# Kernel tuning notes

Hardware: AMD Instinct MI355X
Metric: run time of the kernel (lower is better)

## Reference

```python
import jax, jax.numpy as jnp
import numpy as np

ALPHA = 0.8  # STE clipping threshold (unused in fwd-only path)


def binary_sign(x):
    # torch: x.sign() with zeros mapped to +1 => where(x >= 0, 1, -1)
    return jnp.where(x >= 0, jnp.ones((), x.dtype), -jnp.ones((), x.dtype))


def setup_inputs() -> dict:
    key = jax.random.key(0)
    ks = jax.random.split(key, 5)
    B, D = 16384, 4096
    x = jax.random.normal(ks[0], (B, D), dtype=jnp.float32)
    w0 = jax.random.normal(ks[1], (D, D), dtype=jnp.float32) * 0.1
    w1 = jax.random.normal(ks[2], (D, D), dtype=jnp.float32) * 0.1
    w2 = jax.random.normal(ks[3], (D, D), dtype=jnp.float32) * 0.1
    w3 = jax.random.normal(ks[4], (1, D), dtype=jnp.float32) * 0.1
    b0 = jnp.zeros((D,), jnp.float32)
    b1 = jnp.zeros((D,), jnp.float32)
    b2 = jnp.zeros((D,), jnp.float32)
    b3 = jnp.zeros((1,), jnp.float32)
    return {"x": x, "w0": w0, "b0": b0, "w1": w1, "b1": b1,
            "w2": w2, "b2": b2, "w3": w3, "b3": b3}


def reference(x, w0, b0, w1, b1, w2, b2, w3, b3):
    h = x
    for w, b in ((w0, b0), (w1, b1), (w2, b2), (w3, b3)):
        # BinaryLinear: binarize weights, dense matmul, add bias
        z = jnp.einsum('bi,oi->bo', h, binary_sign(w)) + b
        # BinaryActivation: binarize pre-activation
        h = binary_sign(z)
    return h  # [B, 1]
```

## Files before the change

### kernel.cpp

```cpp
#include <hip/hip_runtime.h>

typedef int   v4i  __attribute__((ext_vector_type(4)));
typedef int   v16i __attribute__((ext_vector_type(16)));
typedef float f4   __attribute__((ext_vector_type(4)));

#define DD 4096
#define BATCH 16384

__device__ __forceinline__ void gload16(const void* g, void* l) {
  __builtin_amdgcn_global_load_lds((const __attribute__((address_space(1))) void*)g,
                                   (__attribute__((address_space(3))) void*)l, 16, 0, 0);
}
#define ASM_VMCNT(n) asm volatile("s_waitcnt vmcnt(" #n ")" ::: "memory")
#define ASM_LGKM0()  asm volatile("s_waitcnt lgkmcnt(0)" ::: "memory")
#define BARF()       asm volatile("s_barrier" ::: "memory")


__global__ void binarize_swz_k(const float* __restrict__ w, unsigned char* __restrict__ o,
                               int swz_on) {
  int T = blockIdx.x * blockDim.x + threadIdx.x;
  int row = T >> 10, rem = T & 1023;
  int kblk = rem >> 4, seg = (rem >> 2) & 3, q = rem & 3;
  f4 v = *(const f4*)(w + (size_t)row * DD + kblk * 64 + seg * 16 + q * 4);
  unsigned int r = 0;
#pragma unroll
  for (int j = 0; j < 4; ++j) {
    unsigned int b = (v[j] >= 0.0f) ? 0x01u : 0xFFu;
    r |= b << (8 * j);
  }
  int slot = swz_on ? (seg ^ ((row >> 1) & 3)) : seg;
  *(unsigned int*)(o + (size_t)row * DD + kblk * 64 + slot * 16 + q * 4) = r;
}

__global__ void rowsum_k(const unsigned char* __restrict__ wb, int* __restrict__ R) {
  int lane = threadIdx.x & 63, wid = threadIdx.x >> 6;
  int row = blockIdx.x * 4 + wid;
  const unsigned char* p = wb + (size_t)row * DD;
  int s = 0;
#pragma unroll
  for (int j = 0; j < 4; ++j) {
    v4i a = *(const v4i*)(p + lane * 16 + j * 1024);
#pragma unroll
    for (int w = 0; w < 4; ++w) {
      unsigned int xa = (unsigned int)a[w];
#pragma unroll
      for (int by = 0; by < 4; ++by)
        s += (int)(signed char)((xa >> (8 * by)) & 255u);
    }
  }
#pragma unroll
  for (int off = 32; off > 0; off >>= 1) s += __shfl_down(s, off);
  if (lane == 0) R[row] = s;
}

__global__ void digitize_k(const float* __restrict__ x, unsigned char* __restrict__ Xd) {
  int T = blockIdx.x * blockDim.x + threadIdx.x;
  int row = T >> 10, rem = T & 1023;
  int kblk = rem >> 4, seg = (rem >> 2) & 3, q = rem & 3;
  f4 v = *(const f4*)(x + (size_t)row * DD + kblk * 64 + seg * 16 + q * 4);
  unsigned int Y[4];
#pragma unroll
  for (int j = 0; j < 4; ++j) {
    int X = (int)(v[j] * 134217728.0f);
    Y[j] = (unsigned int)(X + 1073741824);
  }
  size_t base = (size_t)row * 16384 + (size_t)kblk * 256;
  int r7 = row & 7;
#pragma unroll
  for (int d = 0; d < 4; ++d) {
    unsigned int wv = ((Y[0] >> (8 * d)) & 255u)
                    | (((Y[1] >> (8 * d)) & 255u) << 8)
                    | (((Y[2] >> (8 * d)) & 255u) << 16)
                    | (((Y[3] >> (8 * d)) & 255u) << 24);
    wv ^= 0x80808080u;
    int slot = ((d << 2) | seg) ^ r7;
    *(unsigned int*)(Xd + base + slot * 16 + q * 4) = wv;
  }
}

__global__ __launch_bounds__(256, 2) void gemm0p_k(
    const unsigned char* __restrict__ Xd, const unsigned char* __restrict__ wb,
    const int* __restrict__ R, const float* __restrict__ bias,
    signed char* __restrict__ h1) {
  __shared__ unsigned char As[2][64 * 256];
  __shared__ unsigned char Bs[2][128 * 64];
  const int tid = threadIdx.x, lane = tid & 63, wid = tid >> 6;
  const int wm = wid >> 1, wn = wid & 1;
  const int bid = blockIdx.x;
  const int xcd = bid & 7, sl = bid >> 3;
  const int m0 = ((xcd << 5) + (sl >> 5)) << 6;
  const int n0 = (sl & 31) << 7;

  v16i acc[4][2];
#pragma unroll
  for (int d = 0; d < 4; ++d)
#pragma unroll
    for (int f = 0; f < 2; ++f)
#pragma unroll
      for (int e = 0; e < 16; ++e) acc[d][f][e] = 0;

  auto stage = [&](int bf, int kb) {
#pragma unroll
    for (int i = 0; i < 4; ++i) {
      int c = wid * 4 + i;
      int lrow = c * 4 + (lane >> 4);
      const unsigned char* g = Xd + (size_t)(m0 + lrow) * 16384 + (size_t)kb * 256 + (lane & 15) * 16;
      gload16(g, &As[bf][c * 1024]);
    }
#pragma unroll
    for (int j = 0; j < 2; ++j) {
      int c = wid * 2 + j;
      int lrowB = c * 16 + (lane >> 2);
      const unsigned char* gB = wb + (size_t)(n0 + lrowB) * 4096 + kb * 64 + (lane & 3) * 16;
      gload16(gB, &Bs[bf][c * 1024]);
    }
  };

  const int rl = lane & 31, hi = lane >> 5;
  const int arow = wm * 32 + rl;
  const int r7 = arow & 7;

  stage(0, 0);
  stage(1, 1);
  ASM_VMCNT(6); BARF();
  int cur = 0;
  for (int t = 0; t < 64; ++t) {
    v4i af[2][4], bg[2][2];
#pragma unroll
    for (int kt = 0; kt < 2; ++kt) {
      int g = kt * 2 + hi;
#pragma unroll
      for (int d = 0; d < 4; ++d) {
        int slot = ((d << 2) | g) ^ r7;
        af[kt][d] = *(const v4i*)&As[cur][arow * 256 + slot * 16];
      }
#pragma unroll
      for (int f = 0; f < 2; ++f) {
        int brow = wn * 64 + f * 32 + rl;
        int slotb = g ^ ((brow >> 1) & 3);
        bg[kt][f] = *(const v4i*)&Bs[cur][brow * 64 + slotb * 16];
      }
    }
    ASM_LGKM0(); BARF();
    if (t < 62) stage(cur, t + 2);
    __builtin_amdgcn_s_setprio(1);
#pragma unroll
    for (int kt = 0; kt < 2; ++kt)
#pragma unroll
      for (int d = 0; d < 4; ++d)
#pragma unroll
        for (int f = 0; f < 2; ++f)
          acc[d][f] = __builtin_amdgcn_mfma_i32_32x32x32_i8(af[kt][d], bg[kt][f], acc[d][f], 0, 0, 0);
    __builtin_amdgcn_s_setprio(0);
    if (t < 62) { ASM_VMCNT(6); BARF(); }
    else if (t == 62) { ASM_VMCNT(0); BARF(); }
    cur ^= 1;
  }

#pragma unroll
  for (int f = 0; f < 2; ++f) {
    int col = n0 + wn * 64 + f * 32 + (lane & 31);
    long long rterm = 1082163328LL * (long long)R[col];
    double bb = (double)bias[col];
#pragma unroll
    for (int r = 0; r < 16; ++r) {
      long long Z = (long long)acc[0][f][r] + 256LL * (long long)acc[1][f][r]
                  + 65536LL * (long long)acc[2][f][r] + 16777216LL * (long long)acc[3][f][r]
                  + rterm;
      double z = (double)Z * 7.450580596923828125e-9 + bb;
      int row = m0 + wm * 32 + (r & 3) + 8 * (r >> 2) + 4 * (lane >> 5);
      int col2 = col ^ (((row >> 1) & 3) << 4);
      h1[(size_t)row * DD + col2] = (z >= 0.0) ? (signed char)1 : (signed char)(-1);
    }
  }
}

__global__ __launch_bounds__(512, 2) void gemm0f_k(
    const float* __restrict__ x, const unsigned char* __restrict__ wb,
    const int* __restrict__ R, const float* __restrict__ bias,
    signed char* __restrict__ h1) {
  __shared__ signed char As[2][4][128 * 80];
  __shared__ signed char Bs[2][128 * 80];
  const int tid = threadIdx.x;
  const int lane = tid & 63, wid = tid >> 6;
  const int wm = wid >> 1, wn = wid & 1;
  const int n0 = blockIdx.x * 128, m0 = blockIdx.y * 128;

  v16i acc[4][2];
#pragma unroll
  for (int d = 0; d < 4; ++d)
#pragma unroll
    for (int f = 0; f < 2; ++f)
#pragma unroll
      for (int e = 0; e < 16; ++e) acc[d][f][e] = 0;

  const int arow_l = tid >> 4, aseg = tid & 15;
  const int brow = tid >> 2,  bseg = (tid & 3) * 16;
  f4 va[4]; v4i vb;

  auto loadTile = [&](int kpos) {
#pragma unroll
    for (int p = 0; p < 4; ++p)
      va[p] = *(const f4*)(x + (size_t)(m0 + p * 32 + arow_l) * DD + kpos + aseg * 4);
    vb = *(const v4i*)(wb + (size_t)(n0 + brow) * DD + kpos + bseg);
  };
  auto writeTile = [&](int bf) {
#pragma unroll
    for (int p = 0; p < 4; ++p) {
      int row = p * 32 + arow_l;
      unsigned int Y[4];
#pragma unroll
      for (int j = 0; j < 4; ++j) {
        int X = (int)(va[p][j] * 134217728.0f);
        Y[j] = (unsigned int)(X + 1073741824);
      }
#pragma unroll
      for (int k = 0; k < 4; ++k) {
        unsigned int wv = ((Y[0] >> (8 * k)) & 255u) | (((Y[1] >> (8 * k)) & 255u) << 8)
                        | (((Y[2] >> (8 * k)) & 255u) << 16) | (((Y[3] >> (8 * k)) & 255u) << 24);
        wv ^= 0x80808080u;
        *(unsigned int*)&As[bf][k][row * 80 + aseg * 4] = wv;
      }
    }
    *(v4i*)&Bs[bf][brow * 80 + bseg] = vb;
  };

  loadTile(0); writeTile(0);
  __syncthreads();
  for (int t = 0; t < 64; ++t) {
    int cur = t & 1;
    if (t < 63) loadTile((t + 1) * 64);
#pragma unroll
    for (int kt = 0; kt < 2; ++kt) {
      int g = kt * 2 + (lane >> 5);
      int ar = (wm * 32 + (lane & 31)) * 80 + g * 16;
      v4i a[4], b[2];
#pragma unroll
      for (int d = 0; d < 4; ++d) a[d] = *(const v4i*)&As[cur][d][ar];
#pragma unroll
      for (int f = 0; f < 2; ++f) {
        int br = wn * 64 + f * 32 + (lane & 31);
        int slotb = g ^ ((br >> 1) & 3);
        b[f] = *(const v4i*)&Bs[cur][br * 80 + slotb * 16];
      }
#pragma unroll
      for (int d = 0; d < 4; ++d)
#pragma unroll
        for (int f = 0; f < 2; ++f)
          acc[d][f] = __builtin_amdgcn_mfma_i32_32x32x32_i8(a[d], b[f], acc[d][f], 0, 0, 0);
    }
    if (t < 63) writeTile(cur ^ 1);
    __syncthreads();
  }

#pragma unroll
  for (int f = 0; f < 2; ++f) {
    int col = n0 + wn * 64 + f * 32 + (lane & 31);
    long long rterm = 1082163328LL * (long long)R[col];
    double bb = (double)bias[col];
#pragma unroll
    for (int r = 0; r < 16; ++r) {
      long long Z = (long long)acc[0][f][r] + 256LL * (long long)acc[1][f][r]
                  + 65536LL * (long long)acc[2][f][r] + 16777216LL * (long long)acc[3][f][r]
                  + rterm;
      double z = (double)Z * 7.450580596923828125e-9 + bb;
      int row = m0 + wm * 32 + (r & 3) + 8 * (r >> 2) + 4 * (lane >> 5);
      int col2 = col ^ (((row >> 1) & 3) << 4);
      h1[(size_t)row * DD + col2] = (z >= 0.0) ? (signed char)1 : (signed char)(-1);
    }
  }
}

__global__ __launch_bounds__(256, 3) void gemm_bin_k(
    const unsigned char* __restrict__ A, const unsigned char* __restrict__ Bw,
    const float* __restrict__ bias, signed char* __restrict__ out) {
  __shared__ unsigned char As[2][128 * 64];
  __shared__ unsigned char Bs[2][128 * 64];
  const int tid = threadIdx.x, lane = tid & 63, wid = tid >> 6;
  const int wm = wid >> 1, wn = wid & 1;
  const int bid = blockIdx.x;
  const int xcd = bid & 7, sl = bid >> 3;
  const int m0 = ((xcd << 4) + (sl >> 5)) << 7;
  const int n0 = (sl & 31) << 7;

  v16i acc[2][2];
#pragma unroll
  for (int mi = 0; mi < 2; ++mi)
#pragma unroll
    for (int f = 0; f < 2; ++f)
#pragma unroll
      for (int e = 0; e < 16; ++e) acc[mi][f][e] = 0;

  auto stage = [&](int bf, int kb) {
#pragma unroll
    for (int j = 0; j < 2; ++j) {
      int c = wid * 2 + j;
      int lrow = c * 16 + (lane >> 2);
      const unsigned char* gA = A  + (size_t)(m0 + lrow) * 4096 + kb * 64 + (lane & 3) * 16;
      const unsigned char* gB = Bw + (size_t)(n0 + lrow) * 4096 + kb * 64 + (lane & 3) * 16;
      gload16(gA, &As[bf][c * 1024]);
      gload16(gB, &Bs[bf][c * 1024]);
    }
  };

  const int rl = lane & 31, hi = lane >> 5;

  stage(0, 0);
  stage(1, 1);
  ASM_VMCNT(4); BARF();
  int cur = 0;
  for (int t = 0; t < 64; ++t) {
    v4i af[2][2], bg[2][2];
#pragma unroll
    for (int kt = 0; kt < 2; ++kt) {
      int g = kt * 2 + hi;
#pragma unroll
      for (int mi = 0; mi < 2; ++mi) {
        int arow = wm * 64 + mi * 32 + rl;
        int slot = g ^ ((arow >> 1) & 3);
        af[kt][mi] = *(const v4i*)&As[cur][arow * 64 + slot * 16];
      }
#pragma unroll
      for (int f = 0; f < 2; ++f) {
        int brow = wn * 64 + f * 32 + rl;
        int slot = g ^ ((brow >> 1) & 3);
        bg[kt][f] = *(const v4i*)&Bs[cur][brow * 64 + slot * 16];
      }
    }
    ASM_LGKM0(); BARF();
    if (t < 62) stage(cur, t + 2);
    __builtin_amdgcn_s_setprio(1);
#pragma unroll
    for (int kt = 0; kt < 2; ++kt)
#pragma unroll
      for (int mi = 0; mi < 2; ++mi)
#pragma unroll
        for (int f = 0; f < 2; ++f)
          acc[mi][f] = __builtin_amdgcn_mfma_i32_32x32x32_i8(af[kt][mi], bg[kt][f], acc[mi][f], 0, 0, 0);
    __builtin_amdgcn_s_setprio(0);
    if (t < 62) { ASM_VMCNT(4); BARF(); }
    else if (t == 62) { ASM_VMCNT(0); BARF(); }
    cur ^= 1;
  }

#pragma unroll
  for (int mi = 0; mi < 2; ++mi)
#pragma unroll
    for (int f = 0; f < 2; ++f) {
      int col = n0 + wn * 64 + f * 32 + (lane & 31);
      float bb = bias[col];
#pragma unroll
      for (int r = 0; r < 16; ++r) {
        float z = (float)acc[mi][f][r] + bb;
        int row = m0 + wm * 64 + mi * 32 + (r & 3) + 8 * (r >> 2) + 4 * (lane >> 5);
        int col2 = col ^ (((row >> 1) & 3) << 4);
        out[(size_t)row * DD + col2] = (z >= 0.0f) ? (signed char)1 : (signed char)(-1);
      }
    }
}

__global__ void final_k(const unsigned char* __restrict__ h, const unsigned char* __restrict__ w3b,
                        const float* __restrict__ b3, float* __restrict__ out) {
  int lane = threadIdx.x & 63, wid = threadIdx.x >> 6;
  int row = blockIdx.x * 4 + wid;
  int swz = ((row >> 1) & 3) << 4;
  const unsigned char* p = h + (size_t)row * DD;
  int s = 0;
#pragma unroll
  for (int j = 0; j < 4; ++j) {
    int e = lane * 16 + j * 1024;
    v4i a = *(const v4i*)(p + (e ^ swz));
    v4i b = *(const v4i*)(w3b + e);
#pragma unroll
    for (int w = 0; w < 4; ++w) {
      unsigned int xa = (unsigned int)a[w], xb = (unsigned int)b[w];
#pragma unroll
      for (int by = 0; by < 4; ++by)
        s += (int)(signed char)((xa >> (8 * by)) & 255u)
           * (int)(signed char)((xb >> (8 * by)) & 255u);
    }
  }
#pragma unroll
  for (int off = 32; off > 0; off >>= 1) s += __shfl_down(s, off);
  if (lane == 0) {
    float z = (float)s + b3[0];
    out[row] = (z >= 0.0f) ? 1.0f : -1.0f;
  }
}

extern "C" void kernel_launch(void* const* d_in, const int* in_sizes, int n_in,
                              void* d_out, int out_size, void* d_ws, size_t ws_size,
                              hipStream_t stream) {
  (void)in_sizes; (void)n_in; (void)out_size;
  const float* x  = (const float*)d_in[0];
  const float* w0 = (const float*)d_in[1];
  const float* b0 = (const float*)d_in[2];
  const float* w1 = (const float*)d_in[3];
  const float* b1 = (const float*)d_in[4];
  const float* w2 = (const float*)d_in[5];
  const float* b2 = (const float*)d_in[6];
  const float* w3 = (const float*)d_in[7];
  const float* b3 = (const float*)d_in[8];

  char* ws = (char*)d_ws;
  unsigned char* w0b = (unsigned char*)(ws + 0);
  unsigned char* w1b = (unsigned char*)(ws + (16ull << 20));
  unsigned char* w2b = (unsigned char*)(ws + (32ull << 20));
  unsigned char* w3b = (unsigned char*)(ws + (48ull << 20));
  int*           R   = (int*)(ws + (48ull << 20) + 65536);
  unsigned char* h1  = (unsigned char*)(ws + (64ull << 20));
  unsigned char* h2  = (unsigned char*)(ws + (128ull << 20));
  unsigned char* Xd  = (unsigned char*)(ws + (128ull << 20));
  float* out = (float*)d_out;

  binarize_swz_k<<<16384, 256, 0, stream>>>(w0, w0b, 1);
  binarize_swz_k<<<16384, 256, 0, stream>>>(w1, w1b, 1);
  binarize_swz_k<<<16384, 256, 0, stream>>>(w2, w2b, 1);
  binarize_swz_k<<<4,     256, 0, stream>>>(w3, w3b, 0);
  rowsum_k<<<1024, 256, 0, stream>>>(w0b, R);

  if (ws_size >= (384ull << 20)) {
    digitize_k<<<65536, 256, 0, stream>>>(x, Xd);
    gemm0p_k<<<8192, 256, 0, stream>>>(Xd, w0b, R, b0, (signed char*)h1);
  } else {
    gemm0f_k<<<dim3(32, 128), 512, 0, stream>>>(x, w0b, R, b0, (signed char*)h1);
  }
  gemm_bin_k<<<4096, 256, 0, stream>>>(h1, w1b, b1, (signed char*)h2);
  gemm_bin_k<<<4096, 256, 0, stream>>>(h2, w2b, b2, (signed char*)h1);
  final_k<<<4096, 256, 0, stream>>>(h1, w3b, b3, out);
}
```

Before: 1.927 ms.

## Triple-buffer LDS in binary GEMM kernels to use one barrier per K-step

Both int8 GEMM kernels move from a double-buffered to a triple-buffered shared-memory pipeline. Each iteration now has a single vmcnt wait and barrier, then issues the next global-to-LDS stage into the buffer computed on the previous step, then runs the MFMA block. This drops the second barrier and the lgkmcnt wait that sat between the LDS reads and the stage issue, so loads can overlap compute more freely. The cost is 1.5x the LDS footprint per block, which may limit occupancy, and the setprio hints around the MFMA block are removed.

New measurement: 2.384 ms. 1.24x slower.

```diff
diff --git a/kernel.cpp b/kernel.cpp
--- a/kernel.cpp
+++ b/kernel.cpp
@@ -12,7 +12,6 @@
                                    (__attribute__((address_space(3))) void*)l, 16, 0, 0);
 }
 #define ASM_VMCNT(n) asm volatile("s_waitcnt vmcnt(" #n ")" ::: "memory")
-#define ASM_LGKM0()  asm volatile("s_waitcnt lgkmcnt(0)" ::: "memory")
 #define BARF()       asm volatile("s_barrier" ::: "memory")
 
 
@@ -82,8 +81,8 @@
     const unsigned char* __restrict__ Xd, const unsigned char* __restrict__ wb,
     const int* __restrict__ R, const float* __restrict__ bias,
     signed char* __restrict__ h1) {
-  __shared__ unsigned char As[2][64 * 256];
-  __shared__ unsigned char Bs[2][128 * 64];
+  __shared__ __align__(16) unsigned char As[3][64 * 256];
+  __shared__ __align__(16) unsigned char Bs[3][128 * 64];
   const int tid = threadIdx.x, lane = tid & 63, wid = tid >> 6;
   const int wm = wid >> 1, wn = wid & 1;
   const int bid = blockIdx.x;
@@ -120,11 +119,7 @@
   const int arow = wm * 32 + rl;
   const int r7 = arow & 7;
 
-  stage(0, 0);
-  stage(1, 1);
-  ASM_VMCNT(6); BARF();
-  int cur = 0;
-  for (int t = 0; t < 64; ++t) {
+  auto compute = [&](int cur) {
     v4i af[2][4], bg[2][2];
 #pragma unroll
     for (int kt = 0; kt < 2; ++kt) {
@@ -141,9 +136,6 @@
         bg[kt][f] = *(const v4i*)&Bs[cur][brow * 64 + slotb * 16];
       }
     }
-    ASM_LGKM0(); BARF();
-    if (t < 62) stage(cur, t + 2);
-    __builtin_amdgcn_s_setprio(1);
 #pragma unroll
     for (int kt = 0; kt < 2; ++kt)
 #pragma unroll
@@ -151,11 +143,21 @@
 #pragma unroll
         for (int f = 0; f < 2; ++f)
           acc[d][f] = __builtin_amdgcn_mfma_i32_32x32x32_i8(af[kt][d], bg[kt][f], acc[d][f], 0, 0, 0);
-    __builtin_amdgcn_s_setprio(0);
-    if (t < 62) { ASM_VMCNT(6); BARF(); }
-    else if (t == 62) { ASM_VMCNT(0); BARF(); }
-    cur ^= 1;
-  }
+  };
+
+  stage(0, 0);
+  stage(1, 1);
+  int cur = 0;
+  for (int t = 0; t < 62; ++t) {
+    ASM_VMCNT(6); BARF();
+    int st = cur >= 1 ? cur - 1 : 2;
+    stage(st, t + 2);
+    compute(cur);
+    cur = cur < 2 ? cur + 1 : 0;
+  }
+  ASM_VMCNT(6); BARF(); compute(cur);
+  cur = cur < 2 ? cur + 1 : 0;
+  ASM_VMCNT(0); BARF(); compute(cur);
 
 #pragma unroll
   for (int f = 0; f < 2; ++f) {
@@ -274,8 +276,8 @@
 __global__ __launch_bounds__(256, 3) void gemm_bin_k(
     const unsigned char* __restrict__ A, const unsigned char* __restrict__ Bw,
     const float* __restrict__ bias, signed char* __restrict__ out) {
-  __shared__ unsigned char As[2][128 * 64];
-  __shared__ unsigned char Bs[2][128 * 64];
+  __shared__ __align__(16) unsigned char As[3][128 * 64];
+  __shared__ __align__(16) unsigned char Bs[3][128 * 64];
   const int tid = threadIdx.x, lane = tid & 63, wid = tid >> 6;
   const int wm = wid >> 1, wn = wid & 1;
   const int bid = blockIdx.x;
@@ -305,11 +307,7 @@
 
   const int rl = lane & 31, hi = lane >> 5;
 
-  stage(0, 0);
-  stage(1, 1);
-  ASM_VMCNT(4); BARF();
-  int cur = 0;
-  for (int t = 0; t < 64; ++t) {
+  auto compute = [&](int cur) {
     v4i af[2][2], bg[2][2];
 #pragma unroll
     for (int kt = 0; kt < 2; ++kt) {
@@ -327,9 +325,6 @@
         bg[kt][f] = *(const v4i*)&Bs[cur][brow * 64 + slot * 16];
       }
     }
-    ASM_LGKM0(); BARF();
-    if (t < 62) stage(cur, t + 2);
-    __builtin_amdgcn_s_setprio(1);
 #pragma unroll
     for (int kt = 0; kt < 2; ++kt)
 #pragma unroll
@@ -337,11 +332,21 @@
 #pragma unroll
         for (int f = 0; f < 2; ++f)
           acc[mi][f] = __builtin_amdgcn_mfma_i32_32x32x32_i8(af[kt][mi], bg[kt][f], acc[mi][f], 0, 0, 0);
-    __builtin_amdgcn_s_setprio(0);
-    if (t < 62) { ASM_VMCNT(4); BARF(); }
-    else if (t == 62) { ASM_VMCNT(0); BARF(); }
-    cur ^= 1;
-  }
+  };
+
+  stage(0, 0);
+  stage(1, 1);
+  int cur = 0;
+  for (int t = 0; t < 62; ++t) {
+    ASM_VMCNT(4); BARF();
+    int st = cur >= 1 ? cur - 1 : 2;
+    stage(st, t + 2);
+    compute(cur);
+    cur = cur < 2 ? cur + 1 : 0;
+  }
+  ASM_VMCNT(4); BARF(); compute(cur);
+  cur = cur < 2 ? cur + 1 : 0;
+  ASM_VMCNT(0); BARF(); compute(cur);
 
 #pragma unroll
   for (int mi = 0; mi < 2; ++mi)
```
